# Kernel tuning notes

Measured on AMD Instinct MI355X. Metric: run time of the kernel, lower is better.

Reference implementation:

```python
import jax, jax.numpy as jnp
import numpy as np

NUM_NODES = 100000
NUM_EDGES = 3200000
D_IN, D_HID, D_OUT = 64, 64, 32


def setup_inputs() -> dict:
    key = jax.random.key(0)
    k1, k2, k3, k4, k5 = jax.random.split(key, 5)
    edge_index = jax.random.randint(k1, (2, NUM_EDGES), 0, NUM_NODES, dtype=jnp.int64)
    edge_weight = jax.random.uniform(k2, (NUM_EDGES,), dtype=jnp.float32)
    emb = jax.random.normal(k3, (NUM_NODES, D_IN), dtype=jnp.float32)
    # glorot-ish scaled weights for the two GCNConv layers
    W1 = jax.random.normal(k4, (D_IN, D_HID), dtype=jnp.float32) * (1.0 / np.sqrt(D_IN))
    b1 = jnp.zeros((D_HID,), dtype=jnp.float32)
    W2 = jax.random.normal(k5, (D_HID, D_OUT), dtype=jnp.float32) * (1.0 / np.sqrt(D_HID))
    b2 = jnp.zeros((D_OUT,), dtype=jnp.float32)
    return {"edge_index": edge_index, "edge_weight": edge_weight,
            "emb": emb, "W1": W1, "b1": b1, "W2": W2, "b2": b2}


def reference(edge_index, edge_weight, emb, W1, b1, W2, b2):
    N = emb.shape[0]
    row, col = edge_index[0], edge_index[1]
    # PyG gcn_norm: add self-loops (weight 1.0), symmetric normalization
    loop = jnp.arange(N, dtype=edge_index.dtype)
    row_f = jnp.concatenate([row, loop])
    col_f = jnp.concatenate([col, loop])
    ew_f = jnp.concatenate([edge_weight, jnp.ones((N,), dtype=edge_weight.dtype)])
    deg = jax.ops.segment_sum(ew_f, col_f, num_segments=N)          # [N]
    deg_inv_sqrt = jnp.where(deg > 0, jax.lax.rsqrt(deg), 0.0)      # inf -> 0
    norm = deg_inv_sqrt[row_f] * ew_f * deg_inv_sqrt[col_f]         # [E+N]

    def gcn_conv(x, W, b):
        x = x @ W                                                    # [N, d_out]
        msg = x[row_f] * norm[:, None]                               # [E+N, d_out]
        out = jax.ops.segment_sum(msg, col_f, num_segments=N)       # [N, d_out]
        return out + b

    x = jax.nn.relu(gcn_conv(emb, W1, b1))
    x = gcn_conv(x, W2, b2)
    # F.normalize(p=2, dim=1, eps=1e-12)
    l2 = jnp.linalg.norm(x, axis=1, keepdims=True)
    return x / jnp.maximum(l2, 1e-12)
```

## Files before the change

kernel.cpp:

```cpp
#include <hip/hip_runtime.h>
#include <hip/hip_fp16.h>
#include <math.h>

#define THREADS 256
#define BWIDTH 512
#define BSHIFT 9
#define CHUNK 3125
#define G1ROWS 16
#define G2ROWS 16

__global__ void init_kernel(const int* __restrict__ ei32, int* __restrict__ flag,
                            unsigned int* __restrict__ gcnt) {
    int t = threadIdx.x;
    gcnt[t] = 0u;
    if (t == 0) {
        int z = (ei32[1] == 0) + (ei32[3] == 0) + (ei32[5] == 0) + (ei32[7] == 0);
        *flag = (z == 4) ? 1 : 0;
    }
}

__device__ __forceinline__ int edge_at(const void* ei, int is64, size_t idx) {
    return is64 ? (int)((const long long*)ei)[idx] : ((const int*)ei)[idx];
}

__device__ __forceinline__ float wdec(unsigned int v) {
    return __half2float(__ushort_as_half((unsigned short)(v & 0x7FFFu)));
}

__device__ __forceinline__ void acc8(float* acc, float w, int4 g) {
    float2 x0 = __half22float2(*(const __half2*)&g.x);
    float2 x1 = __half22float2(*(const __half2*)&g.y);
    float2 x2 = __half22float2(*(const __half2*)&g.z);
    float2 x3 = __half22float2(*(const __half2*)&g.w);
    acc[0] = fmaf(w, x0.x, acc[0]); acc[1] = fmaf(w, x0.y, acc[1]);
    acc[2] = fmaf(w, x1.x, acc[2]); acc[3] = fmaf(w, x1.y, acc[3]);
    acc[4] = fmaf(w, x2.x, acc[4]); acc[5] = fmaf(w, x2.y, acc[5]);
    acc[6] = fmaf(w, x3.x, acc[6]); acc[7] = fmaf(w, x3.y, acc[7]);
}

__global__ void p1_count_kernel(const void* __restrict__ ei, const int* __restrict__ flag,
                                unsigned int* __restrict__ gcnt, unsigned int* __restrict__ table,
                                int E, int B) {
    __shared__ unsigned int lcnt[256];
    int t = threadIdx.x, b = blockIdx.x;
    lcnt[t] = 0u;
    __syncthreads();
    int is64 = *flag;
    int base = b * CHUNK;
    int end = min(E, base + CHUNK);
    for (int e = base + t; e < end; e += THREADS) {
        int c = edge_at(ei, is64, (size_t)E + e);
        atomicAdd(&lcnt[c >> BSHIFT], 1u);
    }
    __syncthreads();
    if (t < B) table[(size_t)b * 256 + t] = atomicAdd(&gcnt[t], lcnt[t]);
}

__global__ void p2_scan_kernel(const unsigned int* __restrict__ gcnt,
                               unsigned int* __restrict__ bstart, int B, int E) {
    int t = threadIdx.x;
    unsigned int v = (t < B) ? gcnt[t] : 0u;
    unsigned int incl = v;
    int lane = t & 63, wid = t >> 6;
#pragma unroll
    for (int off = 1; off < 64; off <<= 1) {
        unsigned int x = __shfl_up(incl, off);
        if (lane >= off) incl += x;
    }
    __shared__ unsigned int ws4[4];
    if (lane == 63) ws4[wid] = incl;
    __syncthreads();
    unsigned int wb = 0;
    for (int w = 0; w < wid; ++w) wb += ws4[w];
    unsigned int excl = wb + incl - v;
    if (t < B) bstart[t] = excl;
    if (t == 0) bstart[B] = (unsigned int)E;
}

__global__ void p3_scatter_kernel(const void* __restrict__ ei, const float* __restrict__ ew,
                                  const int* __restrict__ flag,
                                  const unsigned int* __restrict__ bstart,
                                  const unsigned int* __restrict__ table,
                                  int2* __restrict__ out, int E, int B) {
    __shared__ int2 stage[CHUNK];
    __shared__ unsigned char lbin[CHUNK];
    __shared__ unsigned short perm[CHUNK];
    __shared__ unsigned int lcnt[256];
    __shared__ unsigned int lcur[256];
    __shared__ int shiftb[256];
    __shared__ unsigned int ws4[4];

    int t = threadIdx.x, b = blockIdx.x;
    lcnt[t] = 0u;
    __syncthreads();
    int is64 = *flag;
    int base = b * CHUNK;
    int end = min(E, base + CHUNK);
    int n = end - base;
    for (int i = t; i < n; i += THREADS) {
        int e = base + i;
        int r = edge_at(ei, is64, (size_t)e);
        int c = edge_at(ei, is64, (size_t)E + e);
        int bin = c >> BSHIFT;
        stage[i] = make_int2(r | ((c & (BWIDTH - 1)) << 17), __float_as_int(ew[e]));
        lbin[i] = (unsigned char)bin;
        atomicAdd(&lcnt[bin], 1u);
    }
    __syncthreads();
    unsigned int v = lcnt[t];
    unsigned int incl = v;
    int lane = t & 63, wid = t >> 6;
#pragma unroll
    for (int off = 1; off < 64; off <<= 1) {
        unsigned int x = __shfl_up(incl, off);
        if (lane >= off) incl += x;
    }
    if (lane == 63) ws4[wid] = incl;
    __syncthreads();
    unsigned int wb = 0;
    for (int w = 0; w < wid; ++w) wb += ws4[w];
    unsigned int excl = wb + incl - v;
    lcur[t] = excl;
    shiftb[t] = (t < B) ? ((int)(bstart[t] + table[(size_t)b * 256 + t]) - (int)excl) : 0;
    __syncthreads();
    for (int i = t; i < n; i += THREADS) {
        unsigned int pos = atomicAdd(&lcur[lbin[i]], 1u);
        perm[pos] = (unsigned short)i;
    }
    __syncthreads();
    for (int k = t; k < n; k += THREADS) {
        int i = perm[k];
        int bin = lbin[i];
        out[(size_t)(shiftb[bin] + k)] = stage[i];
    }
}

__global__ void p5_bucket_kernel(const int2* __restrict__ bucketed,
                                 const unsigned int* __restrict__ bstart,
                                 float* __restrict__ dinv, int* __restrict__ colptr,
                                 unsigned int* __restrict__ csrp, int N, int E) {
    __shared__ unsigned int cnt[BWIDTH];
    __shared__ float deg[BWIDTH];
    __shared__ unsigned int cur[BWIDTH];
    __shared__ unsigned int ws4[4];

    int t = threadIdx.x, b = blockIdx.x;
    cnt[t] = 0u; cnt[t + 256] = 0u;
    deg[t] = 0.f; deg[t + 256] = 0.f;
    __syncthreads();
    unsigned int s = bstart[b], e2 = bstart[b + 1];
    for (unsigned int j = s + t; j < e2; j += THREADS) {
        int2 v = bucketed[j];
        unsigned int cl = ((unsigned int)v.x) >> 17;
        atomicAdd(&cnt[cl], 1u);
        atomicAdd(&deg[cl], __int_as_float(v.y));
    }
    __syncthreads();
    unsigned int a0 = cnt[2 * t], a1 = cnt[2 * t + 1];
    unsigned int sum = a0 + a1;
    unsigned int incl = sum;
    int lane = t & 63, wid = t >> 6;
#pragma unroll
    for (int off = 1; off < 64; off <<= 1) {
        unsigned int x = __shfl_up(incl, off);
        if (lane >= off) incl += x;
    }
    if (lane == 63) ws4[wid] = incl;
    __syncthreads();
    unsigned int wb = 0;
    for (int w = 0; w < wid; ++w) wb += ws4[w];
    unsigned int exclT = wb + incl - sum;
    unsigned int e0 = exclT, e1 = exclT + a0;
    int node0 = b << BSHIFT;
    int n0 = node0 + 2 * t, n1 = n0 + 1;
    float d0 = rsqrtf(deg[2 * t] + 1.0f);
    float d1 = rsqrtf(deg[2 * t + 1] + 1.0f);
    if (n0 < N) { colptr[n0] = (int)(s + e0); dinv[n0] = d0; }
    if (n1 < N) { colptr[n1] = (int)(s + e1); dinv[n1] = d1; }
    deg[2 * t] = d0;
    deg[2 * t + 1] = d1;
    cur[2 * t] = s + e0;
    cur[2 * t + 1] = s + e1;
    __syncthreads();
    for (unsigned int j = s + t; j < e2; j += THREADS) {
        int2 v = bucketed[j];
        unsigned int cl = ((unsigned int)v.x) >> 17;
        unsigned int pos = atomicAdd(&cur[cl], 1u);
        float w = __int_as_float(v.y) * deg[cl];
        unsigned short hb = __half_as_ushort(__float2half_rn(w));
        csrp[pos] = (((unsigned int)v.x & 0x1FFFFu) << 15) | (unsigned int)(hb & 0x7FFFu);
    }
    if (b == 0 && t == 0) colptr[N] = E;
}

__global__ void gemm1_kernel(const float* __restrict__ X, const float* __restrict__ W,
                             const float* __restrict__ dinv, __half* __restrict__ Y,
                             int N, int tiles) {
    __shared__ float Wl[64 * 64];
    __shared__ float Xl[G1ROWS * 64];
    int tid = threadIdx.x;
    for (int i = tid; i < 64 * 64; i += 256) Wl[i] = W[i];
    int wid = tid >> 6, c = tid & 63;
    __syncthreads();
    for (int tile = blockIdx.x; tile < tiles; tile += gridDim.x) {
        int base = tile * G1ROWS;
        for (int i = tid; i < G1ROWS * 64; i += 256) {
            int rr = base + (i >> 6);
            Xl[i] = (rr < N) ? X[(size_t)rr * 64 + (i & 63)] : 0.f;
        }
        __syncthreads();
#pragma unroll
        for (int rg = 0; rg < G1ROWS / 4; ++rg) {
            int r = rg * 4 + wid;
            int row = base + r;
            if (row < N) {
                float acc = 0.f;
#pragma unroll
                for (int k = 0; k < 64; ++k) acc = fmaf(Xl[r * 64 + k], Wl[k * 64 + c], acc);
                Y[(size_t)row * 64 + c] = __float2half(acc * dinv[row]);
            }
        }
        __syncthreads();
    }
}

__global__ void gemm2_kernel(const __half* __restrict__ H, const float* __restrict__ W,
                             const float* __restrict__ dinv, __half* __restrict__ Y,
                             int N, int tiles) {
    __shared__ float Wl[64 * 32];
    __shared__ float Xl[G2ROWS * 64];
    int tid = threadIdx.x;
    for (int i = tid; i < 64 * 32; i += 256) Wl[i] = W[i];
    int rg0 = tid >> 5, c = tid & 31;
    __syncthreads();
    for (int tile = blockIdx.x; tile < tiles; tile += gridDim.x) {
        int base = tile * G2ROWS;
        for (int i = tid; i < G2ROWS * 32; i += 256) {
            int rr = base + (i >> 5);
            int kk = (i & 31) << 1;
            float2 f = make_float2(0.f, 0.f);
            if (rr < N) f = __half22float2(*(const __half2*)(H + (size_t)rr * 64 + kk));
            Xl[(i >> 5) * 64 + kk] = f.x;
            Xl[(i >> 5) * 64 + kk + 1] = f.y;
        }
        __syncthreads();
#pragma unroll
        for (int rg = 0; rg < G2ROWS / 8; ++rg) {
            int r = rg * 8 + rg0;
            int row = base + r;
            if (row < N) {
                float acc = 0.f;
#pragma unroll
                for (int k = 0; k < 64; ++k) acc = fmaf(Xl[r * 64 + k], Wl[k * 32 + c], acc);
                Y[(size_t)row * 32 + c] = __float2half(acc * dinv[row]);
            }
        }
        __syncthreads();
    }
}

__global__ void agg1_kernel(const __half* __restrict__ X1, const int* __restrict__ colptr,
                            const unsigned int* __restrict__ csrp,
                            const float* __restrict__ dinv, const float* __restrict__ bias,
                            __half* __restrict__ H, int N) {
    int tid = threadIdx.x;
    int node = blockIdx.x * 4 + (tid >> 6);
    if (node >= N) return;
    int lane = tid & 63;
    int eo = lane >> 3;
    int dq = lane & 7;
    int s = colptr[node], e = colptr[node + 1];
    float acc[8] = {0.f, 0.f, 0.f, 0.f, 0.f, 0.f, 0.f, 0.f};
    int j = s;
    while (j + 16 <= e) {
        unsigned int v0 = __builtin_nontemporal_load(&csrp[j + eo]);
        unsigned int v1 = __builtin_nontemporal_load(&csrp[j + 8 + eo]);
        int r0 = (int)(v0 >> 15), r1 = (int)(v1 >> 15);
        int4 g0 = *(const int4*)(X1 + ((size_t)r0 << 6) + (dq << 3));
        int4 g1 = *(const int4*)(X1 + ((size_t)r1 << 6) + (dq << 3));
        acc8(acc, wdec(v0), g0);
        acc8(acc, wdec(v1), g1);
        j += 16;
    }
    for (; j < e; j += 8) {
        int jj = j + eo;
        unsigned int v = (jj < e) ? csrp[jj] : 0u;
        float w = (jj < e) ? wdec(v) : 0.f;
        int r = (int)(v >> 15);
        int4 g = *(const int4*)(X1 + ((size_t)r << 6) + (dq << 3));
        acc8(acc, w, g);
    }
#pragma unroll
    for (int k = 0; k < 8; ++k) {
        acc[k] += __shfl_xor(acc[k], 8);
        acc[k] += __shfl_xor(acc[k], 16);
        acc[k] += __shfl_xor(acc[k], 32);
    }
    if (eo == 0) {
        float di = dinv[node];
        int4 gs = *(const int4*)(X1 + ((size_t)node << 6) + (dq << 3));
        float4 b0 = *(const float4*)(bias + dq * 8);
        float4 b1 = *(const float4*)(bias + dq * 8 + 4);
        float2 x0 = __half22float2(*(const __half2*)&gs.x);
        float2 x1 = __half22float2(*(const __half2*)&gs.y);
        float2 x2 = __half22float2(*(const __half2*)&gs.z);
        float2 x3 = __half22float2(*(const __half2*)&gs.w);
        float a0 = fmaxf(b0.x + fmaf(di, x0.x, acc[0]), 0.f);
        float a1 = fmaxf(b0.y + fmaf(di, x0.y, acc[1]), 0.f);
        float a2 = fmaxf(b0.z + fmaf(di, x1.x, acc[2]), 0.f);
        float a3 = fmaxf(b0.w + fmaf(di, x1.y, acc[3]), 0.f);
        float a4 = fmaxf(b1.x + fmaf(di, x2.x, acc[4]), 0.f);
        float a5 = fmaxf(b1.y + fmaf(di, x2.y, acc[5]), 0.f);
        float a6 = fmaxf(b1.z + fmaf(di, x3.x, acc[6]), 0.f);
        float a7 = fmaxf(b1.w + fmaf(di, x3.y, acc[7]), 0.f);
        int4 o;
        *(__half2*)&o.x = __floats2half2_rn(a0, a1);
        *(__half2*)&o.y = __floats2half2_rn(a2, a3);
        *(__half2*)&o.z = __floats2half2_rn(a4, a5);
        *(__half2*)&o.w = __floats2half2_rn(a6, a7);
        *(int4*)(H + ((size_t)node << 6) + (dq << 3)) = o;
    }
}

__global__ void agg2_kernel(const __half* __restrict__ X2, const int* __restrict__ colptr,
                            const unsigned int* __restrict__ csrp,
                            const float* __restrict__ dinv, const float* __restrict__ bias,
                            float* __restrict__ out, int N) {
    int tid = threadIdx.x;
    int node = blockIdx.x * 4 + (tid >> 6);
    if (node >= N) return;
    int lane = tid & 63;
    int eo = lane >> 2;
    int dq = lane & 3;
    int s = colptr[node], e = colptr[node + 1];
    float acc[8] = {0.f, 0.f, 0.f, 0.f, 0.f, 0.f, 0.f, 0.f};
    int j = s;
    while (j + 16 <= e) {
        unsigned int v = __builtin_nontemporal_load(&csrp[j + eo]);
        int r = (int)(v >> 15);
        int4 g = *(const int4*)(X2 + ((size_t)r << 5) + (dq << 3));
        acc8(acc, wdec(v), g);
        j += 16;
    }
    if (j < e) {
        int jj = j + eo;
        unsigned int v = (jj < e) ? csrp[jj] : 0u;
        float w = (jj < e) ? wdec(v) : 0.f;
        int r = (int)(v >> 15);
        int4 g = *(const int4*)(X2 + ((size_t)r << 5) + (dq << 3));
        acc8(acc, w, g);
    }
#pragma unroll
    for (int k = 0; k < 8; ++k) {
        acc[k] += __shfl_xor(acc[k], 4);
        acc[k] += __shfl_xor(acc[k], 8);
        acc[k] += __shfl_xor(acc[k], 16);
        acc[k] += __shfl_xor(acc[k], 32);
    }
    float a[8];
    float ss = 0.f;
    {
        float di = dinv[node];
        int4 gs = *(const int4*)(X2 + ((size_t)node << 5) + (dq << 3));
        float4 b0 = *(const float4*)(bias + dq * 8);
        float4 b1 = *(const float4*)(bias + dq * 8 + 4);
        float2 x0 = __half22float2(*(const __half2*)&gs.x);
        float2 x1 = __half22float2(*(const __half2*)&gs.y);
        float2 x2 = __half22float2(*(const __half2*)&gs.z);
        float2 x3 = __half22float2(*(const __half2*)&gs.w);
        a[0] = b0.x + fmaf(di, x0.x, acc[0]);
        a[1] = b0.y + fmaf(di, x0.y, acc[1]);
        a[2] = b0.z + fmaf(di, x1.x, acc[2]);
        a[3] = b0.w + fmaf(di, x1.y, acc[3]);
        a[4] = b1.x + fmaf(di, x2.x, acc[4]);
        a[5] = b1.y + fmaf(di, x2.y, acc[5]);
        a[6] = b1.z + fmaf(di, x3.x, acc[6]);
        a[7] = b1.w + fmaf(di, x3.y, acc[7]);
#pragma unroll
        for (int k = 0; k < 8; ++k) ss = fmaf(a[k], a[k], ss);
    }
    ss += __shfl_xor(ss, 1);
    ss += __shfl_xor(ss, 2);
    float inv = 1.f / fmaxf(sqrtf(ss), 1e-12f);
    if (eo == 0) {
        float4 o0 = make_float4(a[0] * inv, a[1] * inv, a[2] * inv, a[3] * inv);
        float4 o1 = make_float4(a[4] * inv, a[5] * inv, a[6] * inv, a[7] * inv);
        *(float4*)(out + ((size_t)node << 5) + (dq << 3)) = o0;
        *(float4*)(out + ((size_t)node << 5) + (dq << 3) + 4) = o1;
    }
}

extern "C" void kernel_launch(void* const* d_in, const int* in_sizes, int n_in,
                              void* d_out, int out_size, void* d_ws, size_t ws_size,
                              hipStream_t stream) {
    const void* ei = d_in[0];
    const float* ew = (const float*)d_in[1];
    const float* emb = (const float*)d_in[2];
    const float* W1 = (const float*)d_in[3];
    const float* b1 = (const float*)d_in[4];
    const float* W2 = (const float*)d_in[5];
    const float* b2 = (const float*)d_in[6];
    float* outp = (float*)d_out;

    int E = in_sizes[0] / 2;
    int N = in_sizes[2] / 64;
    int B = (N + BWIDTH - 1) >> BSHIFT;
    int GP = (E + CHUNK - 1) / CHUNK;

    char* p = (char*)d_ws;
    auto alloc = [&](size_t bytes) {
        void* q = (void*)p;
        p += (bytes + 255) & ~(size_t)255;
        return q;
    };
    unsigned int* gcnt   = (unsigned int*)alloc(256 * 4);
    unsigned int* bstart = (unsigned int*)alloc(257 * 4);
    int*          flag   = (int*)alloc(256);
    unsigned int* table  = (unsigned int*)alloc((size_t)GP * 256 * 4);
    int2*   bucketed = (int2*)alloc((size_t)E * 8);
    unsigned int* csrp = (unsigned int*)alloc(((size_t)E + 64) * 4);
    float*  dinv     = (float*)alloc((size_t)N * 4);
    int*    colptr   = (int*)alloc(((size_t)N + 1) * 4);
    __half* X1h      = (__half*)alloc((size_t)N * 64 * 2);
    __half* H        = (__half*)alloc((size_t)N * 64 * 2);
    __half* X2h      = X1h;

    int tiles1 = (N + G1ROWS - 1) / G1ROWS;
    int tiles2 = (N + G2ROWS - 1) / G2ROWS;

    init_kernel<<<1, 256, 0, stream>>>((const int*)ei, flag, gcnt);
    p1_count_kernel<<<GP, THREADS, 0, stream>>>(ei, flag, gcnt, table, E, B);
    p2_scan_kernel<<<1, 256, 0, stream>>>(gcnt, bstart, B, E);
    p3_scatter_kernel<<<GP, THREADS, 0, stream>>>(ei, ew, flag, bstart, table,
                                                  bucketed, E, B);
    p5_bucket_kernel<<<B, THREADS, 0, stream>>>(bucketed, bstart, dinv, colptr, csrp, N, E);
    gemm1_kernel<<<1024, THREADS, 0, stream>>>(emb, W1, dinv, X1h, N, tiles1);
    agg1_kernel<<<(N + 3) / 4, THREADS, 0, stream>>>(X1h, colptr, csrp, dinv, b1, H, N);
    gemm2_kernel<<<1024, THREADS, 0, stream>>>(H, W2, dinv, X2h, N, tiles2);
    agg2_kernel<<<(N + 3) / 4, THREADS, 0, stream>>>(X2h, colptr, csrp, dinv, b2, outp, N);
}
```

Measured before the change: 292.0 us.

## Scatter edges directly to bucket slots and enlarge per-block chunk

Rewrites the bucket scatter kernel so each thread claims its output slot with a shared-memory atomic on a per-bin cursor and writes straight to global memory. This removes the LDS staging, the local prefix scan and the permutation pass. The chunk per block grows fourfold, so there are fewer blocks and less per-block overhead. In exchange, global writes are no longer grouped by bin within a block, so they are less coalesced. The per-block histogram table presumably has to be produced with the same chunk size elsewhere.

```diff
diff --git a/kernel.cpp b/kernel.cpp
--- a/kernel.cpp
+++ b/kernel.cpp
@@ -5,7 +5,7 @@
 #define THREADS 256
 #define BWIDTH 512
 #define BSHIFT 9
-#define CHUNK 3125
+#define CHUNK 12500
 #define G1ROWS 16
 #define G2ROWS 16
 
@@ -82,56 +82,19 @@
                                   const unsigned int* __restrict__ bstart,
                                   const unsigned int* __restrict__ table,
                                   int2* __restrict__ out, int E, int B) {
-    __shared__ int2 stage[CHUNK];
-    __shared__ unsigned char lbin[CHUNK];
-    __shared__ unsigned short perm[CHUNK];
-    __shared__ unsigned int lcnt[256];
     __shared__ unsigned int lcur[256];
-    __shared__ int shiftb[256];
-    __shared__ unsigned int ws4[4];
-
     int t = threadIdx.x, b = blockIdx.x;
-    lcnt[t] = 0u;
+    lcur[t] = (t < B) ? (bstart[t] + table[(size_t)b * 256 + t]) : 0u;
     __syncthreads();
     int is64 = *flag;
     int base = b * CHUNK;
     int end = min(E, base + CHUNK);
-    int n = end - base;
-    for (int i = t; i < n; i += THREADS) {
-        int e = base + i;
+    for (int e = base + t; e < end; e += THREADS) {
         int r = edge_at(ei, is64, (size_t)e);
         int c = edge_at(ei, is64, (size_t)E + e);
         int bin = c >> BSHIFT;
-        stage[i] = make_int2(r | ((c & (BWIDTH - 1)) << 17), __float_as_int(ew[e]));
-        lbin[i] = (unsigned char)bin;
-        atomicAdd(&lcnt[bin], 1u);
-    }
-    __syncthreads();
-    unsigned int v = lcnt[t];
-    unsigned int incl = v;
-    int lane = t & 63, wid = t >> 6;
-#pragma unroll
-    for (int off = 1; off < 64; off <<= 1) {
-        unsigned int x = __shfl_up(incl, off);
-        if (lane >= off) incl += x;
-    }
-    if (lane == 63) ws4[wid] = incl;
-    __syncthreads();
-    unsigned int wb = 0;
-    for (int w = 0; w < wid; ++w) wb += ws4[w];
-    unsigned int excl = wb + incl - v;
-    lcur[t] = excl;
-    shiftb[t] = (t < B) ? ((int)(bstart[t] + table[(size_t)b * 256 + t]) - (int)excl) : 0;
-    __syncthreads();
-    for (int i = t; i < n; i += THREADS) {
-        unsigned int pos = atomicAdd(&lcur[lbin[i]], 1u);
-        perm[pos] = (unsigned short)i;
-    }
-    __syncthreads();
-    for (int k = t; k < n; k += THREADS) {
-        int i = perm[k];
-        int bin = lbin[i];
-        out[(size_t)(shiftb[bin] + k)] = stage[i];
+        unsigned int pos = atomicAdd(&lcur[bin], 1u);
+        out[pos] = make_int2(r | ((c & (BWIDTH - 1)) << 17), __float_as_int(ew[e]));
     }
 }
 
```

Result: slower. 306.6 us (+5.0%).
